# Kernel optimization log

Hardware: AMD Instinct MI355X
Metric: run time of the kernel (lower is better)

Reference implementation:

```python
import jax, jax.numpy as jnp
import numpy as np

B, F, D = 4096, 64, 512
RED = 4
K = 8


def setup_inputs() -> dict:
    key = jax.random.key(0)
    k1, k2, k3 = jax.random.split(key, 3)
    x = jax.random.normal(k1, (B, F, D), dtype=jnp.float32)
    fan1 = 1.0 / np.sqrt(F)
    fan2 = 1.0 / np.sqrt(F // RED)
    w1 = jax.random.uniform(k2, (F // RED, F), dtype=jnp.float32, minval=-fan1, maxval=fan1)
    b1 = jnp.zeros((F // RED,), dtype=jnp.float32)
    w2 = jax.random.uniform(k3, (F, F // RED), dtype=jnp.float32, minval=-fan2, maxval=fan2)
    b2 = jnp.zeros((F,), dtype=jnp.float32)
    return {"x": x, "w1": w1, "b1": b1, "w2": w2, "b2": b2}


def reference(x, w1, b1, w2, b2):
    # AdaptiveAvgPool1d(1): mean over feature axis -> [B, F]
    pooled = jnp.mean(x, axis=2)
    # 1x1 convs over channel (frame) axis == linear layers
    h = jax.nn.relu(jnp.einsum('bf,rf->br', pooled, w1) + b1)
    weights = jax.nn.sigmoid(jnp.einsum('br,fr->bf', h, w2) + b2)  # [B, F]
    # weights.mean(dim=2) on [B,F,1] is just weights; topk over frames
    _, indices = jax.lax.top_k(weights, K)  # [B, K]
    # gather selected frames: [B, K, D]
    selected = jnp.take_along_axis(x, indices[:, :, None], axis=1)
    return selected
```

## Files before the change

### kernel.cpp

```cpp
#include <hip/hip_runtime.h>
#include <math.h>

#define BB 4096
#define FF 64
#define RR 16
#define DD 512
#define KK 8

typedef float f32x4 __attribute__((ext_vector_type(4)));

__global__ __launch_bounds__(256) void ca1d_fused(
    const float* __restrict__ x,
    const float* __restrict__ w1,
    const float* __restrict__ b1,
    const float* __restrict__ w2,
    const float* __restrict__ b2,
    float* __restrict__ out)
{
    const int b    = blockIdx.x;
    const int tid  = threadIdx.x;
    const int lane = tid & 63;
    const int wave = tid >> 6;

    __shared__ double s_pooled[FF];
    __shared__ double s_h[RR];
    __shared__ double s_z[FF];
    __shared__ float  s_w[FF];
    __shared__ int    s_idx[KK];

    const float* xb = x + (size_t)b * FF * DD;

    #pragma unroll 4
    for (int f = wave; f < FF; f += 4) {
        const float4* row = reinterpret_cast<const float4*>(xb + f * DD);
        float4 v0 = row[lane];
        float4 v1 = row[lane + 64];
        double s = ((double)v0.x + (double)v0.y) + ((double)v0.z + (double)v0.w)
                 + ((double)v1.x + (double)v1.y) + ((double)v1.z + (double)v1.w);
        #pragma unroll
        for (int off = 32; off > 0; off >>= 1)
            s += __shfl_xor(s, off, 64);
        if (lane == 0) s_pooled[f] = s * (1.0 / DD);
    }
    __syncthreads();

    if (tid < RR) {
        double acc = (double)b1[tid];
        const float* wr = w1 + tid * FF;
        #pragma unroll
        for (int f = 0; f < FF; ++f) acc += s_pooled[f] * (double)wr[f];
        s_h[tid] = acc > 0.0 ? acc : 0.0;
    }
    __syncthreads();

    if (tid < FF) {
        double acc = (double)b2[tid];
        const float* wf = w2 + tid * RR;
        #pragma unroll
        for (int r = 0; r < RR; ++r) acc += s_h[r] * (double)wf[r];
        s_z[tid] = acc;
    }
    __syncthreads();

    if (wave == 0) {
        float e   = (float)exp(-s_z[lane]);
        float den = 1.0f + e;
        float v   = 1.0f / den;
        s_w[lane] = v;
        int rank = 0;
        #pragma unroll
        for (int j = 0; j < FF; ++j) {
            float wj = s_w[j];
            rank += (wj > v || (wj == v && j < lane)) ? 1 : 0;
        }
        if (rank < KK) s_idx[rank] = lane;
    }
    __syncthreads();

    f32x4* ob = (f32x4*)(out + (size_t)b * KK * DD);
    #pragma unroll
    for (int i = tid; i < KK * DD / 4; i += 256) {
        int k = i >> 7;
        int c = i & 127;
        const f32x4* src = (const f32x4*)(xb + (size_t)s_idx[k] * DD);
        __builtin_nontemporal_store(src[c], ob + i);
    }
}

extern "C" void kernel_launch(void* const* d_in, const int* in_sizes, int n_in,
                              void* d_out, int out_size, void* d_ws, size_t ws_size,
                              hipStream_t stream) {
    const float* x  = (const float*)d_in[0];
    const float* w1 = (const float*)d_in[1];
    const float* b1 = (const float*)d_in[2];
    const float* w2 = (const float*)d_in[3];
    const float* b2 = (const float*)d_in[4];
    float* out = (float*)d_out;

    ca1d_fused<<<BB, 256, 0, stream>>>(x, w1, b1, w2, b2, out);
}
```

Baseline: 114.6 us.

## Keep frame rows in registers and write selected frames from them

Each wave now loads all 16 of its frame rows into registers with nontemporal loads before reducing, instead of loading one row per iteration. The top-k step stores each frame's rank, and the output is written directly from the register-held rows whose rank is below K. This avoids re-reading the selected rows from global memory and raises the number of loads in flight. In exchange it uses many more VGPRs, which may limit occupancy; the launch bounds hint now asks for 2 blocks per CU.

```diff
diff --git a/kernel.cpp b/kernel.cpp
--- a/kernel.cpp
+++ b/kernel.cpp
@@ -9,7 +9,7 @@
 
 typedef float f32x4 __attribute__((ext_vector_type(4)));
 
-__global__ __launch_bounds__(256) void ca1d_fused(
+__global__ __launch_bounds__(256, 2) void ca1d_fused(
     const float* __restrict__ x,
     const float* __restrict__ w1,
     const float* __restrict__ b1,
@@ -17,26 +17,33 @@
     const float* __restrict__ b2,
     float* __restrict__ out)
 {
+    __shared__ double s_pooled[FF];
+    __shared__ double s_h[RR];
+    __shared__ double s_z[FF];
+    __shared__ float  s_w[FF];
+    __shared__ int    s_rank[FF];
+
     const int b    = blockIdx.x;
     const int tid  = threadIdx.x;
     const int lane = tid & 63;
     const int wave = tid >> 6;
 
-    __shared__ double s_pooled[FF];
-    __shared__ double s_h[RR];
-    __shared__ double s_z[FF];
-    __shared__ float  s_w[FF];
-    __shared__ int    s_idx[KK];
-
     const float* xb = x + (size_t)b * FF * DD;
 
-    #pragma unroll 4
-    for (int f = wave; f < FF; f += 4) {
-        const float4* row = reinterpret_cast<const float4*>(xb + f * DD);
-        float4 v0 = row[lane];
-        float4 v1 = row[lane + 64];
-        double s = ((double)v0.x + (double)v0.y) + ((double)v0.z + (double)v0.w)
-                 + ((double)v1.x + (double)v1.y) + ((double)v1.z + (double)v1.w);
+    f32x4 v0[16], v1[16];
+    #pragma unroll
+    for (int i = 0; i < 16; ++i) {
+        const int f = wave + (i << 2);
+        const f32x4* row = (const f32x4*)(xb + f * DD);
+        v0[i] = __builtin_nontemporal_load(row + lane);
+        v1[i] = __builtin_nontemporal_load(row + lane + 64);
+    }
+
+    #pragma unroll
+    for (int i = 0; i < 16; ++i) {
+        const int f = wave + (i << 2);
+        double s = ((double)v0[i][0] + (double)v0[i][1]) + ((double)v0[i][2] + (double)v0[i][3])
+                 + ((double)v1[i][0] + (double)v1[i][1]) + ((double)v1[i][2] + (double)v1[i][3]);
         #pragma unroll
         for (int off = 32; off > 0; off >>= 1)
             s += __shfl_xor(s, off, 64);
@@ -73,17 +80,20 @@
             float wj = s_w[j];
             rank += (wj > v || (wj == v && j < lane)) ? 1 : 0;
         }
-        if (rank < KK) s_idx[rank] = lane;
+        s_rank[lane] = rank;
     }
     __syncthreads();
 
-    f32x4* ob = (f32x4*)(out + (size_t)b * KK * DD);
+    float* ob = out + (size_t)b * KK * DD;
     #pragma unroll
-    for (int i = tid; i < KK * DD / 4; i += 256) {
-        int k = i >> 7;
-        int c = i & 127;
-        const f32x4* src = (const f32x4*)(xb + (size_t)s_idx[k] * DD);
-        __builtin_nontemporal_store(src[c], ob + i);
+    for (int i = 0; i < 16; ++i) {
+        const int f = wave + (i << 2);
+        const int rk = s_rank[f];
+        if (rk < KK) {
+            f32x4* dst = (f32x4*)(ob + rk * DD);
+            __builtin_nontemporal_store(v0[i], dst + lane);
+            __builtin_nontemporal_store(v1[i], dst + lane + 64);
+        }
     }
 }
 
```

Measured after the change: 129.5 us. 13.0% more time.

## Process two batches per block and overlap MLP/top-k with loads and gather

Applied to the files above, without the earlier changes.

Each block now handles two batch rows, and the grid is halved. Wave 0 runs the small MLP, sigmoid and top-k rank for one batch while all waves pool the next batch, and the other three waves gather the first batch's frames while wave 0 does the second batch's MLP. The aim is to hide the serial single-wave MLP and top-k phase behind memory traffic and to drop some barriers. The cost is fewer blocks in flight and an uneven load across waves during the overlapped phases.

```diff
diff --git a/kernel.cpp b/kernel.cpp
--- a/kernel.cpp
+++ b/kernel.cpp
@@ -6,6 +6,7 @@
 #define RR 16
 #define DD 512
 #define KK 8
+#define NV (KK * DD / 4)
 
 typedef float f32x4 __attribute__((ext_vector_type(4)));
 
@@ -17,74 +18,87 @@
     const float* __restrict__ b2,
     float* __restrict__ out)
 {
-    const int b    = blockIdx.x;
+    __shared__ double s_pooled[2][FF];
+    __shared__ double s_h[2][RR];
+    __shared__ double s_z[2][FF];
+    __shared__ float  s_w[2][FF];
+    __shared__ int    s_idx[2][KK];
+
     const int tid  = threadIdx.x;
     const int lane = tid & 63;
     const int wave = tid >> 6;
 
-    __shared__ double s_pooled[FF];
-    __shared__ double s_h[RR];
-    __shared__ double s_z[FF];
-    __shared__ float  s_w[FF];
-    __shared__ int    s_idx[KK];
+    const size_t b0 = (size_t)blockIdx.x * 2;
+    const float* xA = x + b0 * FF * DD;
+    const float* xB = xA + FF * DD;
 
-    const float* xb = x + (size_t)b * FF * DD;
+    auto stage1 = [&](const float* __restrict__ xb, double* pooled) {
+        #pragma unroll 4
+        for (int f = wave; f < FF; f += 4) {
+            const float4* row = reinterpret_cast<const float4*>(xb + f * DD);
+            float4 v0 = row[lane];
+            float4 v1 = row[lane + 64];
+            double s = ((double)v0.x + (double)v0.y) + ((double)v0.z + (double)v0.w)
+                     + ((double)v1.x + (double)v1.y) + ((double)v1.z + (double)v1.w);
+            #pragma unroll
+            for (int off = 32; off > 0; off >>= 1)
+                s += __shfl_xor(s, off, 64);
+            if (lane == 0) pooled[f] = s * (1.0 / DD);
+        }
+    };
 
-    #pragma unroll 4
-    for (int f = wave; f < FF; f += 4) {
-        const float4* row = reinterpret_cast<const float4*>(xb + f * DD);
-        float4 v0 = row[lane];
-        float4 v1 = row[lane + 64];
-        double s = ((double)v0.x + (double)v0.y) + ((double)v0.z + (double)v0.w)
-                 + ((double)v1.x + (double)v1.y) + ((double)v1.z + (double)v1.w);
-        #pragma unroll
-        for (int off = 32; off > 0; off >>= 1)
-            s += __shfl_xor(s, off, 64);
-        if (lane == 0) s_pooled[f] = s * (1.0 / DD);
-    }
+    auto mlp = [&](int p) {
+        if (lane < RR) {
+            double acc = (double)b1[lane];
+            const float* wr = w1 + lane * FF;
+            #pragma unroll
+            for (int f = 0; f < FF; ++f) acc += s_pooled[p][f] * (double)wr[f];
+            s_h[p][lane] = acc > 0.0 ? acc : 0.0;
+        }
+        {
+            double acc = (double)b2[lane];
+            const float* wf = w2 + lane * RR;
+            #pragma unroll
+            for (int r = 0; r < RR; ++r) acc += s_h[p][r] * (double)wf[r];
+            s_z[p][lane] = acc;
+        }
+        {
+            float e   = (float)exp(-s_z[p][lane]);
+            float den = 1.0f + e;
+            float v   = 1.0f / den;
+            s_w[p][lane] = v;
+            int rank = 0;
+            #pragma unroll
+            for (int j = 0; j < FF; ++j) {
+                float wj = s_w[p][j];
+                rank += (wj > v || (wj == v && j < lane)) ? 1 : 0;
+            }
+            if (rank < KK) s_idx[p][rank] = lane;
+        }
+    };
+
+    auto gather = [&](int p, const float* __restrict__ xb, int t, int nthreads) {
+        f32x4* obv = (f32x4*)(out + (b0 + p) * (size_t)(KK * DD));
+        for (int i = t; i < NV; i += nthreads) {
+            int k = i >> 7;
+            int c = i & 127;
+            const f32x4* src = (const f32x4*)(xb + (size_t)s_idx[p][k] * DD);
+            __builtin_nontemporal_store(src[c], obv + i);
+        }
+    };
+
+    stage1(xA, s_pooled[0]);
     __syncthreads();
 
-    if (tid < RR) {
-        double acc = (double)b1[tid];
-        const float* wr = w1 + tid * FF;
-        #pragma unroll
-        for (int f = 0; f < FF; ++f) acc += s_pooled[f] * (double)wr[f];
-        s_h[tid] = acc > 0.0 ? acc : 0.0;
-    }
+    if (wave == 0) mlp(0);
+    stage1(xB, s_pooled[1]);
     __syncthreads();
 
-    if (tid < FF) {
-        double acc = (double)b2[tid];
-        const float* wf = w2 + tid * RR;
-        #pragma unroll
-        for (int r = 0; r < RR; ++r) acc += s_h[r] * (double)wf[r];
-        s_z[tid] = acc;
-    }
+    if (wave == 0) mlp(1);
+    else gather(0, xA, tid - 64, 192);
     __syncthreads();
 
-    if (wave == 0) {
-        float e   = (float)exp(-s_z[lane]);
-        float den = 1.0f + e;
-        float v   = 1.0f / den;
-        s_w[lane] = v;
-        int rank = 0;
-        #pragma unroll
-        for (int j = 0; j < FF; ++j) {
-            float wj = s_w[j];
-            rank += (wj > v || (wj == v && j < lane)) ? 1 : 0;
-        }
-        if (rank < KK) s_idx[rank] = lane;
-    }
-    __syncthreads();
-
-    f32x4* ob = (f32x4*)(out + (size_t)b * KK * DD);
-    #pragma unroll
-    for (int i = tid; i < KK * DD / 4; i += 256) {
-        int k = i >> 7;
-        int c = i & 127;
-        const f32x4* src = (const f32x4*)(xb + (size_t)s_idx[k] * DD);
-        __builtin_nontemporal_store(src[c], ob + i);
-    }
+    gather(1, xB, tid, 256);
 }
 
 extern "C" void kernel_launch(void* const* d_in, const int* in_sizes, int n_in,
@@ -97,5 +111,5 @@
     const float* b2 = (const float*)d_in[4];
     float* out = (float*)d_out;
 
-    ca1d_fused<<<BB, 256, 0, stream>>>(x, w1, b1, w2, b2, out);
+    ca1d_fused<<<BB / 2, 256, 0, stream>>>(x, w1, b1, w2, b2, out);
 }
```

Result: slower. 141.6 us (+23.6%).
